# Performance work log

Hardware: AMD Instinct MI355X
Metric: run time of the kernel (lower is better)

The kernel has to match this reference:

```python
import jax, jax.numpy as jnp
import numpy as np

H = 12
D_MODEL = 768
D_K = D_MODEL // H  # 64


def setup_inputs() -> dict:
    key = jax.random.key(0)
    ks = jax.random.split(key, 16)
    B, S, D = 4, 1024, D_MODEL
    scale = 1.0 / np.sqrt(D)
    inp = {
        "query": jax.random.normal(ks[0], (B, S, D), jnp.float32),
        "key": jax.random.normal(ks[1], (B, S, D), jnp.float32),
        "value": jax.random.normal(ks[2], (B, S, D), jnp.float32),
        "times": jax.random.normal(ks[3], (2, B, S, D), jnp.float32),
        # learned params (Linear weights stored torch-style [out, in])
        "Wq": jax.random.normal(ks[4], (D, D), jnp.float32) * scale,
        "bq": jnp.zeros((D,), jnp.float32),
        "Wk": jax.random.normal(ks[5], (D, D), jnp.float32) * scale,
        "bk": jnp.zeros((D,), jnp.float32),
        "Wv": jax.random.normal(ks[6], (D, D), jnp.float32) * scale,
        "bv": jnp.zeros((D,), jnp.float32),
        "Wt": jax.random.normal(ks[7], (D, D), jnp.float32) * scale,
        "bt": jnp.zeros((D,), jnp.float32),
        "Wo": jax.random.normal(ks[8], (D, D), jnp.float32) * scale,
        "bo": jnp.zeros((D,), jnp.float32),
    }
    return inp


def _split_heads(x, B, S):
    # [B,S,D] -> [B,H,S,D_K]
    return x.reshape(B, S, H, D_K).transpose(0, 2, 1, 3)


def reference(query, key, value, times, Wq, bq, Wk, bk, Wv, bv, Wt, bt, Wo, bo):
    B, S, D = query.shape
    inv_sqrt_dk = 1.0 / jnp.sqrt(jnp.asarray(D_K, query.dtype))
    # q/k/v projections are identical across time-loop iterations; hoist them.
    q = _split_heads(query @ Wq.T + bq, B, S)   # [B,H,S,dk]
    k = _split_heads(key @ Wk.T + bk, B, S)
    v = _split_heads(value @ Wv.T + bv, B, S)
    x = jnp.zeros_like(q)
    n_times = times.shape[0]
    for i in range(n_times):  # small fixed loop over time embeddings
        t = _split_heads(times[i] @ Wt.T + bt, B, S)
        # dual-score attention: query.time + query.key, each scaled by 1/sqrt(d_k)
        scores = (jnp.einsum('bhqd,bhkd->bhqk', q, t)
                  + jnp.einsum('bhqd,bhkd->bhqk', q, k)) * inv_sqrt_dk
        p = jax.nn.softmax(scores, axis=-1)
        x = x + jnp.einsum('bhqk,bhkd->bhqd', p, v)
    x = x.transpose(0, 2, 1, 3).reshape(B, S, H * D_K)
    return x @ Wo.T + bo
```

## Files before the change

### kernel.cpp

```cpp
#include <hip/hip_runtime.h>
#include <hip/hip_fp16.h>

typedef _Float16 v8h __attribute__((ext_vector_type(8)));
typedef _Float16 v4h __attribute__((ext_vector_type(4)));
typedef _Float16 v2h __attribute__((ext_vector_type(2)));
typedef float v4f __attribute__((ext_vector_type(4)));

#define MFMA_F16 __builtin_amdgcn_mfma_f32_16x16x32_f16
#define EXP2F __builtin_amdgcn_exp2f
#define SCHED_FENCE() __builtin_amdgcn_sched_barrier(0)

__device__ static inline v2h pkrtz(float a, float b) {
  return __builtin_bit_cast(v2h, __builtin_amdgcn_cvt_pkrtz(a, b));
}

__device__ static inline void async_copy16(const void* g, void* l) {
  __builtin_amdgcn_global_load_lds(
      (const __attribute__((address_space(1))) void*)g,
      (__attribute__((address_space(3))) void*)l, 16, 0, 0);
}

struct CastArgs {
  const float* src[5];
  _Float16* dst[5];
  int start[6];
  float scale[5];
};
__global__ void cast_all(CastArgs a) {
  const int g = blockIdx.x * 256 + threadIdx.x;
  if (g >= a.start[5]) return;
  int z = 0;
  #pragma unroll
  for (int i = 1; i < 5; ++i) if (g >= a.start[i]) z = i;
  const int i0 = g - a.start[z];
  const float sc = a.scale[z];
  const float* s = a.src[z] + (size_t)i0 * 8;
  const float4 f0 = *(const float4*)s;
  const float4 f1 = *(const float4*)(s + 4);
  v8h o = {(_Float16)(f0.x * sc), (_Float16)(f0.y * sc),
           (_Float16)(f0.z * sc), (_Float16)(f0.w * sc),
           (_Float16)(f1.x * sc), (_Float16)(f1.y * sc),
           (_Float16)(f1.z * sc), (_Float16)(f1.w * sc)};
  *(v8h*)(a.dst[z] + (size_t)i0 * 8) = o;
}

struct ProjArgs {
  const float* A[5];
  const _Float16* W[5];
  const float* b[5];
  void* out[5];
  float bscale[5];
  int mode[5];
};

__global__ __launch_bounds__(256) void gemm_proj(ProjArgs g) {
  __shared__ _Float16 a_lds[2][128 * 64];
  __shared__ _Float16 w_lds[3][128 * 64];
  const int tid = threadIdx.x;
  const int w = tid >> 6, lane = tid & 63, quad = lane >> 4, l16 = lane & 15;

  const int hw = blockIdx.x + blockIdx.y * 6 + blockIdx.z * 192;
  const int o = (hw & 7) * 120 + (hw >> 3);
  const int n0 = (o % 6) * 128;
  const int m0 = ((o / 6) & 31) * 128;
  const int z = o / 192;

  const float* A = g.A[z];
  const _Float16* W = g.W[z];
  const int wm = (w >> 1) * 64, wn = (w & 1) * 64;

  size_t srcOffW[4]; int ldsOffW[4];
  #pragma unroll
  for (int i = 0; i < 4; ++i) {
    const int c = i * 256 + tid, row = c >> 3, slot = c & 7;
    srcOffW[i] = (size_t)row * 768 + (size_t)((slot ^ (row & 7)) * 8);
    ldsOffW[i] = (i * 256 + w * 64) * 8;
  }
  auto stageW = [&](int kc, int buf) {
    #pragma unroll
    for (int i = 0; i < 4; ++i)
      async_copy16(W + (size_t)n0 * 768 + kc + srcOffW[i],
                   &w_lds[buf][ldsOffW[i]]);
  };

  int rowA[4], colA[4], dstA[4];
  float4 areg[4][2];
  #pragma unroll
  for (int i = 0; i < 4; ++i) {
    const int s = i * 256 + tid, row = s >> 3, slot = s & 7;
    rowA[i] = row;
    colA[i] = (slot ^ (row & 7)) * 8;
    dstA[i] = s * 8;
  }
  auto loadA = [&](int kc) {
    #pragma unroll
    for (int i = 0; i < 4; ++i) {
      const float* p = A + (size_t)(m0 + rowA[i]) * 768 + kc + colA[i];
      areg[i][0] = *(const float4*)p;
      areg[i][1] = *(const float4*)(p + 4);
    }
  };
  auto writeA = [&](int buf) {
    #pragma unroll
    for (int i = 0; i < 4; ++i) {
      const float4 f0 = areg[i][0], f1 = areg[i][1];
      v8h o8 = {(_Float16)f0.x, (_Float16)f0.y, (_Float16)f0.z, (_Float16)f0.w,
                (_Float16)f1.x, (_Float16)f1.y, (_Float16)f1.z, (_Float16)f1.w};
      *(v8h*)&a_lds[buf][dstA[i]] = o8;
    }
  };

  v4f acc[4][4] = {};

  loadA(0);
  stageW(0, 0);
  writeA(0);
  loadA(64);
  stageW(64, 1);
  SCHED_FENCE();
  asm volatile("s_waitcnt vmcnt(12) lgkmcnt(0)" ::: "memory");
  SCHED_FENCE();
  __builtin_amdgcn_s_barrier();
  SCHED_FENCE();

  for (int k = 0; k < 12; ++k) {
    if (k <= 10) writeA((k + 1) & 1);
    if (k <= 9) { loadA((k + 2) * 64); stageW((k + 2) * 64, (k + 2) % 3); }

    const _Float16* al = a_lds[k & 1];
    const _Float16* wl = w_lds[k % 3];
    #pragma unroll
    for (int kh = 0; kh < 2; ++kh) {
      v8h af[4], bf[4];
      #pragma unroll
      for (int mt = 0; mt < 4; ++mt) {
        const int r = wm + mt * 16 + l16;
        af[mt] = *(const v8h*)&al[r * 64 + (((kh * 4 + quad) ^ (r & 7)) * 8)];
      }
      #pragma unroll
      for (int nt = 0; nt < 4; ++nt) {
        const int r = wn + nt * 16 + l16;
        bf[nt] = *(const v8h*)&wl[r * 64 + (((kh * 4 + quad) ^ (r & 7)) * 8)];
      }
      __builtin_amdgcn_s_setprio(1);
      #pragma unroll
      for (int mt = 0; mt < 4; ++mt)
        #pragma unroll
        for (int nt = 0; nt < 4; ++nt)
          acc[mt][nt] = MFMA_F16(af[mt], bf[nt], acc[mt][nt], 0, 0, 0);
      __builtin_amdgcn_s_setprio(0);
    }

    SCHED_FENCE();
    if (k <= 9)
      asm volatile("s_waitcnt vmcnt(12) lgkmcnt(0)" ::: "memory");
    else if (k == 10)
      asm volatile("s_waitcnt vmcnt(0) lgkmcnt(0)" ::: "memory");
    SCHED_FENCE();
    if (k <= 10) { __builtin_amdgcn_s_barrier(); SCHED_FENCE(); }
  }

  const int mode = g.mode[z];
  #pragma unroll
  for (int nt = 0; nt < 4; ++nt) {
    const int col = n0 + wn + nt * 16 + l16;
    const float bv = g.b[z][col] * g.bscale[z];
    if (mode == 1) {
      _Float16* outp = (_Float16*)g.out[z];
      const int h = col >> 6, dk = col & 63;
      #pragma unroll
      for (int mt = 0; mt < 4; ++mt) {
        const int row = m0 + wm + mt * 16 + quad * 4;
        const int b = row >> 10, s = row & 1023;
        const int sp = (s & ~31) | ((s & 12) << 1) | ((s & 16) >> 2);
        v4h pack = {(_Float16)(acc[mt][nt][0] + bv), (_Float16)(acc[mt][nt][1] + bv),
                    (_Float16)(acc[mt][nt][2] + bv), (_Float16)(acc[mt][nt][3] + bv)};
        *(v4h*)&outp[(size_t)((b * 12 + h) * 64 + dk) * 1024 + sp] = pack;
      }
    } else {
      _Float16* outp = (_Float16*)g.out[z];
      #pragma unroll
      for (int mt = 0; mt < 4; ++mt)
        #pragma unroll
        for (int r = 0; r < 4; ++r) {
          const int row = m0 + wm + mt * 16 + quad * 4 + r;
          outp[(size_t)row * 768 + col] = (_Float16)(acc[mt][nt][r] + bv);
        }
    }
  }
}

struct OutArgs { const _Float16* A; const _Float16* W; const float* b; float* out; };

__global__ __launch_bounds__(256) void gemm_out(OutArgs g) {
  __shared__ _Float16 a_lds[2 * 64 * 64];
  __shared__ _Float16 w_lds[2 * 128 * 64];
  const int tid = threadIdx.x;
  const int w = tid >> 6, lane = tid & 63, quad = lane >> 4, l16 = lane & 15;
  const int m0 = blockIdx.x * 64, n0 = blockIdx.y * 128;
  const int wm = (w >> 1) * 32, wn = (w & 1) * 64;

  size_t srcOffW[4]; int ldsOffW[4];
  #pragma unroll
  for (int i = 0; i < 4; ++i) {
    const int c = i * 256 + tid, row = c >> 3, slot = c & 7;
    srcOffW[i] = (size_t)row * 768 + (size_t)((slot ^ (row & 7)) * 8);
    ldsOffW[i] = (i * 256 + w * 64) * 8;
  }
  auto stage = [&](int kc, int buf) {
    #pragma unroll
    for (int i = 0; i < 2; ++i)
      async_copy16(g.A + (size_t)m0 * 768 + kc + srcOffW[i],
                   &a_lds[buf * 4096 + ldsOffW[i]]);
    #pragma unroll
    for (int i = 0; i < 4; ++i)
      async_copy16(g.W + (size_t)n0 * 768 + kc + srcOffW[i],
                   &w_lds[buf * 8192 + ldsOffW[i]]);
  };

  v4f acc[2][4] = {};
  stage(0, 0);

  for (int k0 = 0; k0 < 768; k0 += 64) {
    const int cur = (k0 >> 6) & 1;
    const bool hn = k0 + 64 < 768;
    if (hn) stage(k0 + 64, cur ^ 1);
    SCHED_FENCE();
    if (hn) asm volatile("s_waitcnt vmcnt(6) lgkmcnt(0)" ::: "memory");
    else    asm volatile("s_waitcnt vmcnt(0) lgkmcnt(0)" ::: "memory");
    SCHED_FENCE();
    __builtin_amdgcn_s_barrier();
    SCHED_FENCE();

    const _Float16* al = &a_lds[cur * 4096];
    const _Float16* wl = &w_lds[cur * 8192];
    #pragma unroll
    for (int kh = 0; kh < 2; ++kh) {
      v8h af[2], bf[4];
      #pragma unroll
      for (int mt = 0; mt < 2; ++mt) {
        const int r = wm + mt * 16 + l16;
        af[mt] = *(const v8h*)&al[r * 64 + (((kh * 4 + quad) ^ (r & 7)) * 8)];
      }
      #pragma unroll
      for (int nt = 0; nt < 4; ++nt) {
        const int r = wn + nt * 16 + l16;
        bf[nt] = *(const v8h*)&wl[r * 64 + (((kh * 4 + quad) ^ (r & 7)) * 8)];
      }
      __builtin_amdgcn_s_setprio(1);
      #pragma unroll
      for (int mt = 0; mt < 2; ++mt)
        #pragma unroll
        for (int nt = 0; nt < 4; ++nt)
          acc[mt][nt] = MFMA_F16(af[mt], bf[nt], acc[mt][nt], 0, 0, 0);
      __builtin_amdgcn_s_setprio(0);
    }
    SCHED_FENCE();
    __builtin_amdgcn_s_barrier();
    SCHED_FENCE();
  }

  #pragma unroll
  for (int nt = 0; nt < 4; ++nt) {
    const int col = n0 + wn + nt * 16 + l16;
    const float bv = g.b[col];
    #pragma unroll
    for (int mt = 0; mt < 2; ++mt)
      #pragma unroll
      for (int r = 0; r < 4; ++r) {
        const int row = m0 + wm + mt * 16 + quad * 4 + r;
        g.out[(size_t)row * 768 + col] = acc[mt][nt][r] + bv;
      }
  }
}

__global__ __launch_bounds__(256) void attn(
    const _Float16* __restrict__ Q,
    const _Float16* __restrict__ Kp, const _Float16* __restrict__ T0p,
    const _Float16* __restrict__ T1p,
    const _Float16* __restrict__ Vt,
    _Float16* __restrict__ X)
{
  __shared__ _Float16 lds[6 * 4096];

  const int tid = threadIdx.x;
  const int w = tid >> 6, lane = tid & 63, quad = lane >> 4, l16 = lane & 15;

  const int orig = blockIdx.y * 16 + blockIdx.x;
  const int wgid = (orig & 7) * 96 + (orig >> 3);
  const int bh = wgid >> 4, q0 = (wgid & 15) * 64;
  const int b = bh / 12, h = bh % 12;
  const size_t base = (size_t)b * 1024 * 768 + h * 64;

  const _Float16* ks  = Kp + base;
  const _Float16* t0s = T0p + base;
  const _Float16* t1s = T1p + base;
  const _Float16* vs  = Vt + (size_t)bh * 64 * 1024;

  size_t ktOff[2], vOff[2]; int ldsOff[2];
  #pragma unroll
  for (int i = 0; i < 2; ++i) {
    const int c = i * 256 + w * 64 + lane, row = c >> 3, slot = c & 7;
    const int logical = slot ^ (row & 7);
    ktOff[i] = (size_t)row * 768 + (size_t)(logical * 8);
    vOff[i] = (size_t)row * 1024 + (size_t)(logical * 8);
    ldsOff[i] = c * 8;
  }

  v8h kreg[2], t0reg[2], t1reg[2];
  auto issueLoads = [&](int buf) {
    #pragma unroll
    for (int i = 0; i < 2; ++i) {
      kreg[i]  = *(const v8h*)(ks + ktOff[i]);
      t0reg[i] = *(const v8h*)(t0s + ktOff[i]);
      t1reg[i] = *(const v8h*)(t1s + ktOff[i]);
    }
    #pragma unroll
    for (int i = 0; i < 2; ++i)
      async_copy16(vs + vOff[i], &lds[16384 + buf * 4096 + ldsOff[i]]);
    ks += 64 * 768; t0s += 64 * 768; t1s += 64 * 768; vs += 64;
  };
  auto finishStage = [&](int buf) {
    #pragma unroll
    for (int i = 0; i < 2; ++i) {
      *(v8h*)&lds[buf * 4096 + ldsOff[i]]        = kreg[i] + t0reg[i];
      *(v8h*)&lds[8192 + buf * 4096 + ldsOff[i]] = kreg[i] + t1reg[i];
    }
  };

  const _Float16* Qw = Q + base + (size_t)(q0 + w * 16) * 768;
  const v8h qf0 = *(const v8h*)(Qw + (size_t)l16 * 768 + quad * 8);
  const v8h qf1 = *(const v8h*)(Qw + (size_t)l16 * 768 + 32 + quad * 8);

  int ra0[4], ra1[4];
  #pragma unroll
  for (int t = 0; t < 4; ++t) {
    const int r = t * 16 + l16, rw = r & 7;
    ra0[t] = (r * 64 + ((quad ^ rw) * 8)) * 2;
    ra1[t] = ra0[t] ^ 64;
  }

  const _Float16 one = (_Float16)1.f;
  const v8h ones8 = {one, one, one, one, one, one, one, one};
  v4f o[2][4] = {};
  v4f osum[2] = {};

  issueLoads(0);
  finishStage(0);

  #pragma unroll 2
  for (int cc = 0; cc < 16; ++cc) {
    __syncthreads();
    const int B = (cc & 1) * 8192;
    if (cc < 15) issueLoads((cc + 1) & 1);

    const char* L = (const char*)lds;

    v4f s[2][4];
    __builtin_amdgcn_s_setprio(1);
    #pragma unroll
    for (int kvt = 0; kvt < 4; ++kvt) {
      const v8h k00 = *(const v8h*)(L + B + ra0[kvt]);
      const v8h k01 = *(const v8h*)(L + B + ra1[kvt]);
      const v8h k10 = *(const v8h*)(L + 16384 + B + ra0[kvt]);
      const v8h k11 = *(const v8h*)(L + 16384 + B + ra1[kvt]);
      s[0][kvt] = MFMA_F16(k00, qf0, v4f{}, 0, 0, 0);
      s[0][kvt] = MFMA_F16(k01, qf1, s[0][kvt], 0, 0, 0);
      s[1][kvt] = MFMA_F16(k10, qf0, v4f{}, 0, 0, 0);
      s[1][kvt] = MFMA_F16(k11, qf1, s[1][kvt], 0, 0, 0);
    }
    __builtin_amdgcn_s_setprio(0);

    v8h pb8[2][2];
    #pragma unroll
    for (int t = 0; t < 2; ++t)
      #pragma unroll
      for (int gg = 0; gg < 2; ++gg) {
        const v4f sa = s[t][gg * 2], sb = s[t][gg * 2 + 1];
        const v2h a0 = pkrtz(EXP2F(sa[0]), EXP2F(sa[1]));
        const v2h a1 = pkrtz(EXP2F(sa[2]), EXP2F(sa[3]));
        const v2h b0 = pkrtz(EXP2F(sb[0]), EXP2F(sb[1]));
        const v2h b1 = pkrtz(EXP2F(sb[2]), EXP2F(sb[3]));
        pb8[t][gg] = v8h{a0[0], a0[1], a1[0], a1[1], b0[0], b0[1], b1[0], b1[1]};
        osum[t] = MFMA_F16(ones8, pb8[t][gg], osum[t], 0, 0, 0);
      }

    __builtin_amdgcn_s_setprio(1);
    #pragma unroll
    for (int dkt = 0; dkt < 4; ++dkt) {
      const v8h v0 = *(const v8h*)(L + 32768 + B + ra0[dkt]);
      const v8h v1 = *(const v8h*)(L + 32768 + B + ra1[dkt]);
      o[0][dkt] = MFMA_F16(v0, pb8[0][0], o[0][dkt], 0, 0, 0);
      o[0][dkt] = MFMA_F16(v1, pb8[0][1], o[0][dkt], 0, 0, 0);
      o[1][dkt] = MFMA_F16(v0, pb8[1][0], o[1][dkt], 0, 0, 0);
      o[1][dkt] = MFMA_F16(v1, pb8[1][1], o[1][dkt], 0, 0, 0);
    }
    __builtin_amdgcn_s_setprio(0);

    if (cc < 15) finishStage((cc + 1) & 1);
  }

  const float i0 = 1.0f / osum[0][0], i1 = 1.0f / osum[1][0];

  _Float16* Xw = X + base + (size_t)(q0 + w * 16 + l16) * 768;
  #pragma unroll
  for (int dkt = 0; dkt < 4; ++dkt) {
    v4h pack;
    #pragma unroll
    for (int r = 0; r < 4; ++r)
      pack[r] = (_Float16)(o[0][dkt][r] * i0 + o[1][dkt][r] * i1);
    *(v4h*)&Xw[dkt * 16 + quad * 4] = pack;
  }
}

extern "C" void kernel_launch(void* const* d_in, const int* in_sizes, int n_in,
                              void* d_out, int out_size, void* d_ws, size_t ws_size,
                              hipStream_t stream) {
  const float* query = (const float*)d_in[0];
  const float* key   = (const float*)d_in[1];
  const float* value = (const float*)d_in[2];
  const float* times = (const float*)d_in[3];
  const float* Wq = (const float*)d_in[4];  const float* bq = (const float*)d_in[5];
  const float* Wk = (const float*)d_in[6];  const float* bk = (const float*)d_in[7];
  const float* Wv = (const float*)d_in[8];  const float* bv = (const float*)d_in[9];
  const float* Wt = (const float*)d_in[10]; const float* bt = (const float*)d_in[11];
  const float* Wo = (const float*)d_in[12]; const float* bo = (const float*)d_in[13];
  float* out = (float*)d_out;

  const size_t NELEM = (size_t)4096 * 768;
  const size_t WELEM = (size_t)768 * 768;
  const float QSCALE = 0.125f * 1.4426950408889634f;

  char* ws = (char*)d_ws;
  size_t off = 0;
  auto alloc = [&](size_t bytes) {
    void* p = ws + off; off += (bytes + 255) & ~(size_t)255; return p;
  };
  _Float16* wqh = (_Float16*)alloc(WELEM * 2);
  _Float16* wkh = (_Float16*)alloc(WELEM * 2);
  _Float16* wvh = (_Float16*)alloc(WELEM * 2);
  _Float16* wth = (_Float16*)alloc(WELEM * 2);
  _Float16* woh = (_Float16*)alloc(WELEM * 2);
  _Float16* Qh  = (_Float16*)alloc(NELEM * 2);
  _Float16* Kh  = (_Float16*)alloc(NELEM * 2);
  _Float16* T0h = (_Float16*)alloc(NELEM * 2);
  _Float16* T1h = (_Float16*)alloc(NELEM * 2);
  _Float16* Vt  = (_Float16*)alloc(NELEM * 2);
  _Float16* Xh  = (_Float16*)alloc(NELEM * 2);

  CastArgs ca = {};
  const int nW8 = (int)(WELEM / 8);
  const float* csrc[5] = {Wq, Wk, Wv, Wt, Wo};
  _Float16* cdst[5] = {wqh, wkh, wvh, wth, woh};
  int acc8 = 0;
  for (int i = 0; i < 5; ++i) {
    ca.src[i] = csrc[i]; ca.dst[i] = cdst[i];
    ca.start[i] = acc8;
    acc8 += nW8;
    ca.scale[i] = (i == 0) ? QSCALE : 1.0f;
  }
  ca.start[5] = acc8;
  cast_all<<<dim3((acc8 + 255) / 256), 256, 0, stream>>>(ca);

  ProjArgs pa = {};
  pa.A[0] = key;           pa.W[0] = wkh; pa.b[0] = bk; pa.out[0] = Kh;
  pa.bscale[0] = 1.0f; pa.mode[0] = 0;
  pa.A[1] = times;         pa.W[1] = wth; pa.b[1] = bt; pa.out[1] = T0h;
  pa.bscale[1] = 1.0f; pa.mode[1] = 0;
  pa.A[2] = times + NELEM; pa.W[2] = wth; pa.b[2] = bt; pa.out[2] = T1h;
  pa.bscale[2] = 1.0f; pa.mode[2] = 0;
  pa.A[3] = query;         pa.W[3] = wqh; pa.b[3] = bq; pa.out[3] = Qh;
  pa.bscale[3] = QSCALE; pa.mode[3] = 0;
  pa.A[4] = value;         pa.W[4] = wvh; pa.b[4] = bv; pa.out[4] = Vt;
  pa.bscale[4] = 1.0f; pa.mode[4] = 1;
  gemm_proj<<<dim3(6, 32, 5), 256, 0, stream>>>(pa);

  attn<<<dim3(16, 48), 256, 0, stream>>>(Qh, Kh, T0h, T1h, Vt, Xh);

  OutArgs oa = {Xh, woh, bo, out};
  gemm_out<<<dim3(64, 6), 256, 0, stream>>>(oa);
}
```

Before: 221.1 us.

## Stage fp32 A tiles into LDS asynchronously and convert at fragment load

```diff
diff --git a/kernel.cpp b/kernel.cpp
--- a/kernel.cpp
+++ b/kernel.cpp
@@ -54,8 +54,8 @@
 };
 
 __global__ __launch_bounds__(256) void gemm_proj(ProjArgs g) {
-  __shared__ _Float16 a_lds[2][128 * 64];
-  __shared__ _Float16 w_lds[3][128 * 64];
+  __shared__ float a_lds[128 * 64];
+  __shared__ _Float16 w_lds[128 * 64];
   const int tid = threadIdx.x;
   const int w = tid >> 6, lane = tid & 63, quad = lane >> 4, l16 = lane & 15;
 
@@ -74,73 +74,59 @@
   for (int i = 0; i < 4; ++i) {
     const int c = i * 256 + tid, row = c >> 3, slot = c & 7;
     srcOffW[i] = (size_t)row * 768 + (size_t)((slot ^ (row & 7)) * 8);
-    ldsOffW[i] = (i * 256 + w * 64) * 8;
-  }
-  auto stageW = [&](int kc, int buf) {
+    ldsOffW[i] = c * 8;
+  }
+  size_t srcOffA[8]; int ldsOffA[8];
+  #pragma unroll
+  for (int i = 0; i < 8; ++i) {
+    const int c = i * 256 + tid, row = c >> 4, hp = c & 15;
+    const int hl = hp ^ (row & 15);
+    srcOffA[i] = (size_t)row * 768 + (size_t)(hl * 4);
+    ldsOffA[i] = c * 4;
+  }
+
+  auto stage = [&](int kc) {
+    #pragma unroll
+    for (int i = 0; i < 8; ++i)
+      async_copy16(A + (size_t)m0 * 768 + kc + srcOffA[i], &a_lds[ldsOffA[i]]);
     #pragma unroll
     for (int i = 0; i < 4; ++i)
-      async_copy16(W + (size_t)n0 * 768 + kc + srcOffW[i],
-                   &w_lds[buf][ldsOffW[i]]);
+      async_copy16(W + (size_t)n0 * 768 + kc + srcOffW[i], &w_lds[ldsOffW[i]]);
   };
 
-  int rowA[4], colA[4], dstA[4];
-  float4 areg[4][2];
-  #pragma unroll
-  for (int i = 0; i < 4; ++i) {
-    const int s = i * 256 + tid, row = s >> 3, slot = s & 7;
-    rowA[i] = row;
-    colA[i] = (slot ^ (row & 7)) * 8;
-    dstA[i] = s * 8;
-  }
-  auto loadA = [&](int kc) {
-    #pragma unroll
-    for (int i = 0; i < 4; ++i) {
-      const float* p = A + (size_t)(m0 + rowA[i]) * 768 + kc + colA[i];
-      areg[i][0] = *(const float4*)p;
-      areg[i][1] = *(const float4*)(p + 4);
-    }
-  };
-  auto writeA = [&](int buf) {
-    #pragma unroll
-    for (int i = 0; i < 4; ++i) {
-      const float4 f0 = areg[i][0], f1 = areg[i][1];
-      v8h o8 = {(_Float16)f0.x, (_Float16)f0.y, (_Float16)f0.z, (_Float16)f0.w,
-                (_Float16)f1.x, (_Float16)f1.y, (_Float16)f1.z, (_Float16)f1.w};
-      *(v8h*)&a_lds[buf][dstA[i]] = o8;
-    }
-  };
+  int adrA[4][2][2];
+  #pragma unroll
+  for (int mt = 0; mt < 4; ++mt)
+    #pragma unroll
+    for (int kh = 0; kh < 2; ++kh)
+      #pragma unroll
+      for (int hf = 0; hf < 2; ++hf) {
+        const int r = wm + mt * 16 + l16, sl = kh * 4 + quad;
+        adrA[mt][kh][hf] = r * 256 + (((sl * 2 + hf) ^ (r & 15)) * 16);
+      }
 
   v4f acc[4][4] = {};
 
-  loadA(0);
-  stageW(0, 0);
-  writeA(0);
-  loadA(64);
-  stageW(64, 1);
-  SCHED_FENCE();
-  asm volatile("s_waitcnt vmcnt(12) lgkmcnt(0)" ::: "memory");
-  SCHED_FENCE();
-  __builtin_amdgcn_s_barrier();
-  SCHED_FENCE();
-
   for (int k = 0; k < 12; ++k) {
-    if (k <= 10) writeA((k + 1) & 1);
-    if (k <= 9) { loadA((k + 2) * 64); stageW((k + 2) * 64, (k + 2) % 3); }
-
-    const _Float16* al = a_lds[k & 1];
-    const _Float16* wl = w_lds[k % 3];
+    __syncthreads();
+    stage(k * 64);
+    __syncthreads();
+    const char* aL = (const char*)a_lds;
     #pragma unroll
     for (int kh = 0; kh < 2; ++kh) {
       v8h af[4], bf[4];
       #pragma unroll
       for (int mt = 0; mt < 4; ++mt) {
-        const int r = wm + mt * 16 + l16;
-        af[mt] = *(const v8h*)&al[r * 64 + (((kh * 4 + quad) ^ (r & 7)) * 8)];
+        const v4f fa0 = *(const v4f*)(aL + adrA[mt][kh][0]);
+        const v4f fa1 = *(const v4f*)(aL + adrA[mt][kh][1]);
+        const v2h p0 = pkrtz(fa0[0], fa0[1]), p1 = pkrtz(fa0[2], fa0[3]);
+        const v2h p2 = pkrtz(fa1[0], fa1[1]), p3 = pkrtz(fa1[2], fa1[3]);
+        af[mt] = v8h{p0[0], p0[1], p1[0], p1[1], p2[0], p2[1], p3[0], p3[1]};
       }
       #pragma unroll
       for (int nt = 0; nt < 4; ++nt) {
         const int r = wn + nt * 16 + l16;
-        bf[nt] = *(const v8h*)&wl[r * 64 + (((kh * 4 + quad) ^ (r & 7)) * 8)];
+        bf[nt] = *(const v8h*)&w_lds[r * 64 + (((kh * 4 + quad) ^ (r & 7)) * 8)];
       }
       __builtin_amdgcn_s_setprio(1);
       #pragma unroll
@@ -150,14 +136,6 @@
           acc[mt][nt] = MFMA_F16(af[mt], bf[nt], acc[mt][nt], 0, 0, 0);
       __builtin_amdgcn_s_setprio(0);
     }
-
-    SCHED_FENCE();
-    if (k <= 9)
-      asm volatile("s_waitcnt vmcnt(12) lgkmcnt(0)" ::: "memory");
-    else if (k == 10)
-      asm volatile("s_waitcnt vmcnt(0) lgkmcnt(0)" ::: "memory");
-    SCHED_FENCE();
-    if (k <= 10) { __builtin_amdgcn_s_barrier(); SCHED_FENCE(); }
   }
 
   const int mode = g.mode[z];
```

After: 224.9 us. About the same (+1.7%).

## Shrink projection GEMM pipeline to single A buffer and double W buffer

Applied to the files above, without the earlier changes.

```diff
diff --git a/kernel.cpp b/kernel.cpp
--- a/kernel.cpp
+++ b/kernel.cpp
@@ -54,8 +54,8 @@
 };
 
 __global__ __launch_bounds__(256) void gemm_proj(ProjArgs g) {
-  __shared__ _Float16 a_lds[2][128 * 64];
-  __shared__ _Float16 w_lds[3][128 * 64];
+  __shared__ _Float16 a_lds[128 * 64];
+  __shared__ _Float16 w_lds[2][128 * 64];
   const int tid = threadIdx.x;
   const int w = tid >> 6, lane = tid & 63, quad = lane >> 4, l16 = lane & 15;
 
@@ -100,13 +100,13 @@
       areg[i][1] = *(const float4*)(p + 4);
     }
   };
-  auto writeA = [&](int buf) {
+  auto writeA = [&]() {
     #pragma unroll
     for (int i = 0; i < 4; ++i) {
       const float4 f0 = areg[i][0], f1 = areg[i][1];
       v8h o8 = {(_Float16)f0.x, (_Float16)f0.y, (_Float16)f0.z, (_Float16)f0.w,
                 (_Float16)f1.x, (_Float16)f1.y, (_Float16)f1.z, (_Float16)f1.w};
-      *(v8h*)&a_lds[buf][dstA[i]] = o8;
+      *(v8h*)&a_lds[dstA[i]] = o8;
     }
   };
 
@@ -114,28 +114,31 @@
 
   loadA(0);
   stageW(0, 0);
-  writeA(0);
-  loadA(64);
-  stageW(64, 1);
-  SCHED_FENCE();
-  asm volatile("s_waitcnt vmcnt(12) lgkmcnt(0)" ::: "memory");
-  SCHED_FENCE();
-  __builtin_amdgcn_s_barrier();
-  SCHED_FENCE();
 
   for (int k = 0; k < 12; ++k) {
-    if (k <= 10) writeA((k + 1) & 1);
-    if (k <= 9) { loadA((k + 2) * 64); stageW((k + 2) * 64, (k + 2) % 3); }
-
-    const _Float16* al = a_lds[k & 1];
-    const _Float16* wl = w_lds[k % 3];
+    const int cur = k & 1;
+    const bool hn = k < 11;
+
+    writeA();
+    if (hn) {
+      loadA((k + 1) * 64);
+      stageW((k + 1) * 64, cur ^ 1);
+    }
+    SCHED_FENCE();
+    if (hn) asm volatile("s_waitcnt vmcnt(12) lgkmcnt(0)" ::: "memory");
+    else    asm volatile("s_waitcnt vmcnt(0) lgkmcnt(0)" ::: "memory");
+    SCHED_FENCE();
+    __builtin_amdgcn_s_barrier();
+    SCHED_FENCE();
+
+    const _Float16* wl = w_lds[cur];
     #pragma unroll
     for (int kh = 0; kh < 2; ++kh) {
       v8h af[4], bf[4];
       #pragma unroll
       for (int mt = 0; mt < 4; ++mt) {
         const int r = wm + mt * 16 + l16;
-        af[mt] = *(const v8h*)&al[r * 64 + (((kh * 4 + quad) ^ (r & 7)) * 8)];
+        af[mt] = *(const v8h*)&a_lds[r * 64 + (((kh * 4 + quad) ^ (r & 7)) * 8)];
       }
       #pragma unroll
       for (int nt = 0; nt < 4; ++nt) {
@@ -150,14 +153,9 @@
           acc[mt][nt] = MFMA_F16(af[mt], bf[nt], acc[mt][nt], 0, 0, 0);
       __builtin_amdgcn_s_setprio(0);
     }
-
-    SCHED_FENCE();
-    if (k <= 9)
-      asm volatile("s_waitcnt vmcnt(12) lgkmcnt(0)" ::: "memory");
-    else if (k == 10)
-      asm volatile("s_waitcnt vmcnt(0) lgkmcnt(0)" ::: "memory");
-    SCHED_FENCE();
-    if (k <= 10) { __builtin_amdgcn_s_barrier(); SCHED_FENCE(); }
+    SCHED_FENCE();
+    __builtin_amdgcn_s_barrier();
+    SCHED_FENCE();
   }
 
   const int mode = g.mode[z];
```

Result: slower. 258.3 us (+16.9%).
